# Kernel optimization log

Hardware: AMD Instinct MI355X
Metric: run time of the kernel (lower is better)

The kernel has to match this reference:

```python
import jax, jax.numpy as jnp
import numpy as np

WH, WW = 8, 8          # window size
NH = 8                 # num heads
ED = 256               # embed dim
HD = ED // NH          # head dim
SCALE = HD ** -0.5


def setup_inputs() -> dict:
    key = jax.random.key(0)
    k1, k2, k3, k4 = jax.random.split(key, 4)
    x = jax.random.normal(k1, (8, ED, 128, 128), dtype=jnp.float32)
    w_qkv = jax.random.normal(k2, (3 * ED, ED), dtype=jnp.float32) * (ED ** -0.5)
    w_out = jax.random.normal(k3, (ED, ED), dtype=jnp.float32) * (ED ** -0.5)
    b_out = jax.random.normal(k4, (ED,), dtype=jnp.float32) * 0.01
    return {"x": x, "w_qkv": w_qkv, "w_out": w_out, "b_out": b_out}


def reference(x, w_qkv, w_out, b_out):
    # x: [B, C, H, W] (NCHW) -> [B, H, W, C]
    x = jnp.transpose(x, (0, 2, 3, 1))
    B, H, W, C = x.shape
    pad_h = (WH - H % WH) % WH
    pad_w = (WW - W % WW) % WW
    x = jnp.pad(x, ((0, 0), (0, pad_h), (0, pad_w), (0, 0)))
    Hp, Wp = H + pad_h, W + pad_w
    nh, nw = Hp // WH, Wp // WW
    N = WH * WW
    # window partition -> [B*nh*nw, N, C]
    xw = x.reshape(B, nh, WH, nw, WW, C).transpose(0, 1, 3, 2, 4, 5).reshape(-1, N, C)
    # qkv projection (no bias): [nW, N, 3, NH, HD]
    qkv = (xw @ w_qkv.T).reshape(-1, N, 3, NH, HD)
    q, k, v = qkv[:, :, 0], qkv[:, :, 1], qkv[:, :, 2]  # [nW, N, NH, HD]
    # NOTE: faithful to source — attention across the HEADS axis per token
    attn = jnp.einsum('wnhd,wngd->wnhg', q, k) * SCALE  # [nW, N, NH, NH]
    attn = jax.nn.softmax(attn, axis=-1)
    out = jnp.einsum('wnhg,wngd->wnhd', attn, v)        # [nW, N, NH, HD]
    # torch: transpose(1,2).reshape(-1, N, C)
    out = out.transpose(0, 2, 1, 3).reshape(-1, N, C)
    out = out @ w_out.T + b_out
    # window merge
    out = out.reshape(B, nh, nw, WH, WW, C).transpose(0, 1, 3, 2, 4, 5).reshape(B, Hp, Wp, C)
    out = out[:, :H, :W, :]
    # faithful final permute(0,3,2,1): [B, C, W, H]
    return jnp.transpose(out, (0, 3, 2, 1))
```

## Files before the change

### kernel.cpp

```cpp
#include <hip/hip_runtime.h>

#define SCALE 0.17677669529663687f

typedef __attribute__((ext_vector_type(8))) short bf16x8;
typedef __attribute__((ext_vector_type(4))) float f32x4;

__device__ __forceinline__ unsigned short f2bf(float f) {
    unsigned u = __float_as_uint(f);
    u += 0x7FFFu + ((u >> 16) & 1u);
    return (unsigned short)(u >> 16);
}
__device__ __forceinline__ float bf2f(unsigned short s) {
    return __uint_as_float(((unsigned)s) << 16);
}

__global__ __launch_bounds__(256) void wconv_kernel(
        const float* __restrict__ w_qkv, const float* __restrict__ w_out,
        unsigned short* __restrict__ wq, unsigned short* __restrict__ wo) {
    int idx = blockIdx.x * 256 + threadIdx.x;
    if (idx < 196608) wq[idx] = f2bf(w_qkv[idx]);
    else if (idx < 262144) wo[idx - 196608] = f2bf(w_out[idx - 196608]);
}

__global__ __launch_bounds__(512, 4) void qkv_attn_kernel(
        const float* __restrict__ x, const unsigned short* __restrict__ wq,
        unsigned short* __restrict__ o_ws) {
    __shared__ unsigned char lds[65536];
    const int tid = threadIdx.x;
    const int bid = blockIdx.x;
    const int rpair = bid & 3;
    const int iwp   = (bid >> 2) & 7;
    const int ih    = (bid >> 5) & 15;
    const int b     = bid >> 9;
    const int r0 = rpair * 2;
    const float* xb2 = x + (size_t)b * 4194304 + (size_t)(ih * 8 + r0) * 128 + iwp * 16;

    #pragma unroll
    for (int it = 0; it < 4; ++it) {
        int idx = it * 512 + tid;
        int c_lo = idx & 7;
        int q4   = (idx >> 3) & 3;
        int c_hi = (idx >> 5) & 31;
        int rl   = idx >> 10;
        int c = c_hi * 8 + c_lo;
        float4 v = *(const float4*)(xb2 + (size_t)c * 16384 + rl * 128 + q4 * 4);
        #pragma unroll
        for (int j = 0; j < 4; ++j) {
            int t = rl * 16 + q4 * 4 + j;
            int slot = (c >> 3) ^ (t & 7);
            float f = (j == 0) ? v.x : (j == 1) ? v.y : (j == 2) ? v.z : v.w;
            *(unsigned short*)(lds + 49152 + t * 512 + (slot << 4) + (c & 7) * 2) = f2bf(f);
        }
    }
    __syncthreads();

    const int lane = tid & 63;
    const int wave = tid >> 6;
    const int lrow = lane & 15;
    const int lk   = lane >> 4;

    {
        const int j0 = wave * 96;
        f32x4 acc[2][6];
        #pragma unroll
        for (int mt = 0; mt < 2; ++mt)
            #pragma unroll
            for (int nt = 0; nt < 6; ++nt)
                acc[mt][nt] = (f32x4){0.f, 0.f, 0.f, 0.f};
        #pragma unroll
        for (int k = 0; k < 8; ++k) {
            bf16x8 a[2], bb[6];
            #pragma unroll
            for (int mt = 0; mt < 2; ++mt) {
                int t = mt * 16 + lrow;
                int slot = (k * 4 + lk) ^ (t & 7);
                a[mt] = *(const bf16x8*)(lds + 49152 + t * 512 + (slot << 4));
            }
            #pragma unroll
            for (int nt = 0; nt < 6; ++nt) {
                int j = j0 + nt * 16 + lrow;
                bb[nt] = *(const bf16x8*)((const unsigned char*)wq + (size_t)j * 512 + k * 64 + lk * 16);
            }
            #pragma unroll
            for (int mt = 0; mt < 2; ++mt)
                #pragma unroll
                for (int nt = 0; nt < 6; ++nt)
                    acc[mt][nt] = __builtin_amdgcn_mfma_f32_16x16x32_bf16(a[mt], bb[nt], acc[mt][nt], 0, 0, 0);
        }
        #pragma unroll
        for (int mt = 0; mt < 2; ++mt)
            #pragma unroll
            for (int nt = 0; nt < 6; ++nt)
                #pragma unroll
                for (int i = 0; i < 4; ++i) {
                    int t = mt * 16 + lk * 4 + i;
                    int ch = j0 + nt * 16 + lrow;
                    int slot = (ch >> 3) ^ (t & 7);
                    *(unsigned short*)(lds + t * 1536 + (slot << 4) + (ch & 7) * 2) = f2bf(acc[mt][nt][i]);
                }
    }
    __syncthreads();

    {
        const int t  = tid >> 4;
        const int h  = (tid >> 1) & 7;
        const int hf = tid & 1;
        const int tx = t & 7;
        const unsigned char* row = lds + t * 1536;
        float q[16];
        #pragma unroll
        for (int jj = 0; jj < 2; ++jj) {
            int slot = (h * 4 + hf * 2 + jj) ^ tx;
            bf16x8 v = *(const bf16x8*)(row + (slot << 4));
            #pragma unroll
            for (int e = 0; e < 8; ++e) q[jj * 8 + e] = bf2f((unsigned short)v[e]);
        }
        float dots[8];
        #pragma unroll
        for (int g = 0; g < 8; ++g) {
            float acc = 0.f;
            #pragma unroll
            for (int jj = 0; jj < 2; ++jj) {
                int slot = (32 + g * 4 + hf * 2 + jj) ^ tx;
                bf16x8 v = *(const bf16x8*)(row + (slot << 4));
                #pragma unroll
                for (int e = 0; e < 8; ++e) acc += q[jj * 8 + e] * bf2f((unsigned short)v[e]);
            }
            dots[g] = acc;
        }
        #pragma unroll
        for (int g = 0; g < 8; ++g)
            dots[g] = (dots[g] + __shfl_xor(dots[g], 1, 64)) * SCALE;
        float mx = dots[0];
        #pragma unroll
        for (int g = 1; g < 8; ++g) mx = fmaxf(mx, dots[g]);
        float sum = 0.f;
        #pragma unroll
        for (int g = 0; g < 8; ++g) { dots[g] = __expf(dots[g] - mx); sum += dots[g]; }
        float inv = 1.f / sum;
        float o[16];
        #pragma unroll
        for (int d = 0; d < 16; ++d) o[d] = 0.f;
        #pragma unroll
        for (int g = 0; g < 8; ++g) {
            float p = dots[g] * inv;
            #pragma unroll
            for (int jj = 0; jj < 2; ++jj) {
                int slot = (64 + g * 4 + hf * 2 + jj) ^ tx;
                bf16x8 v = *(const bf16x8*)(row + (slot << 4));
                #pragma unroll
                for (int e = 0; e < 8; ++e) o[jj * 8 + e] += p * bf2f((unsigned short)v[e]);
            }
        }
        const int rl = t >> 4, sg = t & 15;
        const int win = b * 256 + ih * 16 + iwp * 2 + (sg >> 3);
        const int r = r0 + rl, s = sg & 7;
        unsigned short* dst = o_ws + ((size_t)win * 64 + h * 8 + r) * 256 + s * 32 + hf * 16;
        #pragma unroll
        for (int jj = 0; jj < 2; ++jj) {
            bf16x8 pk;
            #pragma unroll
            for (int e = 0; e < 8; ++e) pk[e] = (short)f2bf(o[jj * 8 + e]);
            *(bf16x8*)(dst + jj * 8) = pk;
        }
    }
}

__global__ __launch_bounds__(512, 4) void outproj_kernel(
        const unsigned short* __restrict__ o_ws, const unsigned short* __restrict__ wo,
        const float* __restrict__ b_out, float* __restrict__ out) {
    __shared__ unsigned char lds[65536];
    const int tid = threadIdx.x;
    const int bid = blockIdx.x;
    const int b  = bid >> 8;
    const int ih = (bid >> 4) & 15;
    const int iw = bid & 15;

    {
        const unsigned char* src = (const unsigned char*)(o_ws + (size_t)bid * 16384);
        #pragma unroll
        for (int it = 0; it < 4; ++it) {
            int q = it * 512 + tid;
            int np = q >> 5;
            int slot = (q & 31) ^ (np & 7);
            *(bf16x8*)(lds + np * 512 + (slot << 4)) = *(const bf16x8*)(src + q * 16);
        }
    }
    __syncthreads();

    const int lane = tid & 63;
    const int wave = tid >> 6;
    const int lrow = lane & 15;
    const int lk   = lane >> 4;
    const int j0 = wave * 32;

    f32x4 acc[4][2];
    #pragma unroll
    for (int mt = 0; mt < 4; ++mt)
        #pragma unroll
        for (int nt = 0; nt < 2; ++nt)
            acc[mt][nt] = (f32x4){0.f, 0.f, 0.f, 0.f};
    #pragma unroll
    for (int k = 0; k < 8; ++k) {
        bf16x8 a[4], bb[2];
        #pragma unroll
        for (int mt = 0; mt < 4; ++mt) {
            int t = mt * 16 + lrow;
            int slot = (k * 4 + lk) ^ (t & 7);
            a[mt] = *(const bf16x8*)(lds + t * 512 + (slot << 4));
        }
        #pragma unroll
        for (int nt = 0; nt < 2; ++nt) {
            int j = j0 + nt * 16 + lrow;
            bb[nt] = *(const bf16x8*)((const unsigned char*)wo + (size_t)j * 512 + k * 64 + lk * 16);
        }
        #pragma unroll
        for (int mt = 0; mt < 4; ++mt)
            #pragma unroll
            for (int nt = 0; nt < 2; ++nt)
                acc[mt][nt] = __builtin_amdgcn_mfma_f32_16x16x32_bf16(a[mt], bb[nt], acc[mt][nt], 0, 0, 0);
    }
    float bias[2];
    #pragma unroll
    for (int nt = 0; nt < 2; ++nt) bias[nt] = b_out[j0 + nt * 16 + lrow];
    __syncthreads();
    #pragma unroll
    for (int mt = 0; mt < 4; ++mt)
        #pragma unroll
        for (int nt = 0; nt < 2; ++nt)
            #pragma unroll
            for (int i = 0; i < 4; ++i) {
                int t = mt * 16 + lk * 4 + i;
                int e = j0 + nt * 16 + lrow;
                int sl = (e >> 2) ^ (t & 7);
                *(float*)(lds + t * 1024 + (sl << 4) + (e & 3) * 4) = acc[mt][nt][i] + bias[nt];
            }
    __syncthreads();
    const size_t obase = ((size_t)b * 256) * 16384 + (size_t)(iw * 8) * 128 + ih * 8;
    #pragma unroll
    for (int it = 0; it < 4; ++it) {
        int idx = it * 512 + tid;
        int e = idx >> 3, sp = idx & 7;
        float vals[8];
        #pragma unroll
        for (int rp = 0; rp < 8; ++rp) {
            int t = rp * 8 + sp;
            int sl = (e >> 2) ^ (t & 7);
            vals[rp] = *(const float*)(lds + t * 1024 + (sl << 4) + (e & 3) * 4);
        }
        float* po = out + obase + (size_t)e * 16384 + sp * 128;
        *(float4*)po       = make_float4(vals[0], vals[1], vals[2], vals[3]);
        *(float4*)(po + 4) = make_float4(vals[4], vals[5], vals[6], vals[7]);
    }
}

extern "C" void kernel_launch(void* const* d_in, const int* in_sizes, int n_in,
                              void* d_out, int out_size, void* d_ws, size_t ws_size,
                              hipStream_t stream) {
    const float* x     = (const float*)d_in[0];
    const float* w_qkv = (const float*)d_in[1];
    const float* w_out = (const float*)d_in[2];
    const float* b_out = (const float*)d_in[3];
    float* out = (float*)d_out;

    unsigned short* o_ws = (unsigned short*)d_ws;
    unsigned short* wq   = (unsigned short*)((char*)d_ws + 67108864);
    unsigned short* wo   = wq + 196608;

    wconv_kernel<<<dim3(1024), dim3(256), 0, stream>>>(w_qkv, w_out, wq, wo);
    qkv_attn_kernel<<<dim3(4096), dim3(512), 0, stream>>>(x, wq, o_ws);
    outproj_kernel<<<dim3(2048), dim3(512), 0, stream>>>(o_ws, wo, b_out, out);
}
```

Baseline: 292.0 us.

## Split fused QKV+attention into separate GEMM and attention kernels when workspace allows

When the workspace is large enough, the fused qkv_attn kernel is replaced by a standalone QKV GEMM kernel that writes a bf16 QKV buffer (about 200 MB), followed by a separate per-token attention kernel. The output projection kernel is also reworked to use half the LDS, writing results back in two halves, and its occupancy hint is raised. The intent is higher occupancy and simpler kernels, at the cost of an extra round trip of the large QKV tensor through global memory. The original fused path is kept as a fallback for small workspaces.

```diff
diff --git a/kernel.cpp b/kernel.cpp
--- a/kernel.cpp
+++ b/kernel.cpp
@@ -20,6 +20,266 @@
     int idx = blockIdx.x * 256 + threadIdx.x;
     if (idx < 196608) wq[idx] = f2bf(w_qkv[idx]);
     else if (idx < 262144) wo[idx - 196608] = f2bf(w_out[idx - 196608]);
+}
+
+
+__global__ __launch_bounds__(512, 4) void qkv_gemm_kernel(
+        const float* __restrict__ x, const unsigned short* __restrict__ wq,
+        unsigned short* __restrict__ qkv_ws) {
+    __shared__ unsigned char lds[65536];
+    const int tid = threadIdx.x;
+    const int tb  = blockIdx.x << 6;
+    const int b   = tb >> 14;
+    const int hw  = tb & 16383;
+    const float* xb = x + (size_t)b * 4194304 + hw;
+
+    #pragma unroll
+    for (int it = 0; it < 8; ++it) {
+        int idx = it * 512 + tid;
+        int c = idx >> 4, q4 = idx & 15;
+        float4 v = *(const float4*)(xb + (size_t)c * 16384 + q4 * 4);
+        #pragma unroll
+        for (int j = 0; j < 4; ++j) {
+            int t = q4 * 4 + j;
+            int slot = (c >> 3) ^ (t & 7);
+            float f = (j == 0) ? v.x : (j == 1) ? v.y : (j == 2) ? v.z : v.w;
+            *(unsigned short*)(lds + t * 512 + (slot << 4) + (c & 7) * 2) = f2bf(f);
+        }
+    }
+    __syncthreads();
+
+    const int lane = tid & 63, wave = tid >> 6;
+    const int lrow = lane & 15, lk = lane >> 4;
+    const int j0w = wave * 32;
+
+    for (int nb = 0; nb < 3; ++nb) {
+        f32x4 acc[4][2];
+        #pragma unroll
+        for (int mt = 0; mt < 4; ++mt)
+            #pragma unroll
+            for (int nt = 0; nt < 2; ++nt)
+                acc[mt][nt] = (f32x4){0.f, 0.f, 0.f, 0.f};
+        #pragma unroll
+        for (int k = 0; k < 8; ++k) {
+            bf16x8 a[4], bb[2];
+            #pragma unroll
+            for (int mt = 0; mt < 4; ++mt) {
+                int t = mt * 16 + lrow;
+                int slot = (k * 4 + lk) ^ (t & 7);
+                a[mt] = *(const bf16x8*)(lds + t * 512 + (slot << 4));
+            }
+            #pragma unroll
+            for (int nt = 0; nt < 2; ++nt) {
+                int j = nb * 256 + j0w + nt * 16 + lrow;
+                bb[nt] = *(const bf16x8*)((const unsigned char*)wq + (size_t)j * 512 + k * 64 + lk * 16);
+            }
+            #pragma unroll
+            for (int mt = 0; mt < 4; ++mt)
+                #pragma unroll
+                for (int nt = 0; nt < 2; ++nt)
+                    acc[mt][nt] = __builtin_amdgcn_mfma_f32_16x16x32_bf16(a[mt], bb[nt], acc[mt][nt], 0, 0, 0);
+        }
+        #pragma unroll
+        for (int mt = 0; mt < 4; ++mt)
+            #pragma unroll
+            for (int nt = 0; nt < 2; ++nt)
+                #pragma unroll
+                for (int i = 0; i < 4; ++i) {
+                    int t = mt * 16 + lk * 4 + i;
+                    int ch = j0w + nt * 16 + lrow;
+                    int slot = (ch >> 3) ^ (t & 7);
+                    *(unsigned short*)(lds + 32768 + t * 512 + (slot << 4) + (ch & 7) * 2) = f2bf(acc[mt][nt][i]);
+                }
+        __syncthreads();
+        #pragma unroll
+        for (int it = 0; it < 4; ++it) {
+            int idx = it * 512 + tid;
+            int t = idx >> 5, c = idx & 31;
+            int slot = c ^ (t & 7);
+            bf16x8 vch = *(const bf16x8*)(lds + 32768 + t * 512 + (slot << 4));
+            *(bf16x8*)(qkv_ws + (size_t)(tb + t) * 768 + nb * 256 + c * 8) = vch;
+        }
+        __syncthreads();
+    }
+}
+
+__global__ __launch_bounds__(512, 6) void attn_kernel(
+        const unsigned short* __restrict__ qkv_ws, unsigned short* __restrict__ o_ws) {
+    __shared__ unsigned char lds[49152];
+    const int tid = threadIdx.x;
+    const int tb  = blockIdx.x << 5;
+
+    {
+        const int t = tid >> 4, cpart = tid & 15;
+        const unsigned short* src = qkv_ws + (size_t)(tb + t) * 768;
+        #pragma unroll
+        for (int ci = 0; ci < 6; ++ci) {
+            int c = ci * 16 + cpart;
+            *(bf16x8*)(lds + t * 1536 + ((c ^ (t & 7)) << 4)) = *(const bf16x8*)(src + c * 8);
+        }
+    }
+    __syncthreads();
+
+    const int t  = tid >> 4;
+    const int h  = (tid >> 1) & 7;
+    const int hf = tid & 1;
+    const int tx = t & 7;
+    const unsigned char* row = lds + t * 1536;
+    float q[16];
+    #pragma unroll
+    for (int jj = 0; jj < 2; ++jj) {
+        int slot = (h * 4 + hf * 2 + jj) ^ tx;
+        bf16x8 v = *(const bf16x8*)(row + (slot << 4));
+        #pragma unroll
+        for (int e = 0; e < 8; ++e) q[jj * 8 + e] = bf2f((unsigned short)v[e]);
+    }
+    float dots[8];
+    #pragma unroll
+    for (int g = 0; g < 8; ++g) {
+        float acc = 0.f;
+        #pragma unroll
+        for (int jj = 0; jj < 2; ++jj) {
+            int slot = (32 + g * 4 + hf * 2 + jj) ^ tx;
+            bf16x8 v = *(const bf16x8*)(row + (slot << 4));
+            #pragma unroll
+            for (int e = 0; e < 8; ++e) acc += q[jj * 8 + e] * bf2f((unsigned short)v[e]);
+        }
+        dots[g] = acc;
+    }
+    #pragma unroll
+    for (int g = 0; g < 8; ++g)
+        dots[g] = (dots[g] + __shfl_xor(dots[g], 1, 64)) * SCALE;
+    float mx = dots[0];
+    #pragma unroll
+    for (int g = 1; g < 8; ++g) mx = fmaxf(mx, dots[g]);
+    float sum = 0.f;
+    #pragma unroll
+    for (int g = 0; g < 8; ++g) { dots[g] = __expf(dots[g] - mx); sum += dots[g]; }
+    float inv = 1.f / sum;
+    float o[16];
+    #pragma unroll
+    for (int d = 0; d < 16; ++d) o[d] = 0.f;
+    #pragma unroll
+    for (int g = 0; g < 8; ++g) {
+        float p = dots[g] * inv;
+        #pragma unroll
+        for (int jj = 0; jj < 2; ++jj) {
+            int slot = (64 + g * 4 + hf * 2 + jj) ^ tx;
+            bf16x8 v = *(const bf16x8*)(row + (slot << 4));
+            #pragma unroll
+            for (int e = 0; e < 8; ++e) o[jj * 8 + e] += p * bf2f((unsigned short)v[e]);
+        }
+    }
+    const int tok = tb + t;
+    const int bb2 = tok >> 14, rem = tok & 16383;
+    const int himg = rem >> 7, wimg = rem & 127;
+    const int ih = himg >> 3, r = himg & 7;
+    const int iw = wimg >> 3, s = wimg & 7;
+    const int win = (bb2 << 8) + (ih << 4) + iw;
+    unsigned short* dst = o_ws + ((size_t)win * 64 + h * 8 + r) * 256 + s * 32 + hf * 16;
+    #pragma unroll
+    for (int jj = 0; jj < 2; ++jj) {
+        bf16x8 pk;
+        #pragma unroll
+        for (int e = 0; e < 8; ++e) pk[e] = (short)f2bf(o[jj * 8 + e]);
+        *(bf16x8*)(dst + jj * 8) = pk;
+    }
+}
+
+__global__ __launch_bounds__(512, 6) void outproj_kernel(
+        const unsigned short* __restrict__ o_ws, const unsigned short* __restrict__ wo,
+        const float* __restrict__ b_out, float* __restrict__ out) {
+    __shared__ unsigned char lds[32768];
+    const int tid = threadIdx.x;
+    const int bid = blockIdx.x;
+    const int b  = bid >> 8;
+    const int ih = (bid >> 4) & 15;
+    const int iw = bid & 15;
+
+    {
+        const unsigned char* src = (const unsigned char*)(o_ws + (size_t)bid * 16384);
+        #pragma unroll
+        for (int it = 0; it < 4; ++it) {
+            int q = it * 512 + tid;
+            int np = q >> 5;
+            int slot = (q & 31) ^ (np & 7);
+            *(bf16x8*)(lds + np * 512 + (slot << 4)) = *(const bf16x8*)(src + q * 16);
+        }
+    }
+    __syncthreads();
+
+    const int lane = tid & 63;
+    const int wave = tid >> 6;
+    const int lrow = lane & 15;
+    const int lk   = lane >> 4;
+    const int j0 = wave * 32;
+
+    f32x4 acc[4][2];
+    #pragma unroll
+    for (int mt = 0; mt < 4; ++mt)
+        #pragma unroll
+        for (int nt = 0; nt < 2; ++nt)
+            acc[mt][nt] = (f32x4){0.f, 0.f, 0.f, 0.f};
+    #pragma unroll
+    for (int k = 0; k < 8; ++k) {
+        bf16x8 a[4], bb[2];
+        #pragma unroll
+        for (int mt = 0; mt < 4; ++mt) {
+            int t = mt * 16 + lrow;
+            int slot = (k * 4 + lk) ^ (t & 7);
+            a[mt] = *(const bf16x8*)(lds + t * 512 + (slot << 4));
+        }
+        #pragma unroll
+        for (int nt = 0; nt < 2; ++nt) {
+            int j = j0 + nt * 16 + lrow;
+            bb[nt] = *(const bf16x8*)((const unsigned char*)wo + (size_t)j * 512 + k * 64 + lk * 16);
+        }
+        #pragma unroll
+        for (int mt = 0; mt < 4; ++mt)
+            #pragma unroll
+            for (int nt = 0; nt < 2; ++nt)
+                acc[mt][nt] = __builtin_amdgcn_mfma_f32_16x16x32_bf16(a[mt], bb[nt], acc[mt][nt], 0, 0, 0);
+    }
+    float bias[2];
+    #pragma unroll
+    for (int nt = 0; nt < 2; ++nt) bias[nt] = b_out[j0 + nt * 16 + lrow];
+    __syncthreads();
+
+    const size_t obase = ((size_t)b * 256) * 16384 + (size_t)(iw * 8) * 128 + ih * 8;
+    #pragma unroll
+    for (int half = 0; half < 2; ++half) {
+        if ((wave >> 2) == half) {
+            int jl = (wave & 3) * 32;
+            #pragma unroll
+            for (int mt = 0; mt < 4; ++mt)
+                #pragma unroll
+                for (int nt = 0; nt < 2; ++nt)
+                    #pragma unroll
+                    for (int i = 0; i < 4; ++i) {
+                        int t = mt * 16 + lk * 4 + i;
+                        int el = jl + nt * 16 + lrow;
+                        int sl = (el >> 2) ^ (t & 7);
+                        *(float*)(lds + t * 512 + (sl << 4) + (el & 3) * 4) = acc[mt][nt][i] + bias[nt];
+                    }
+        }
+        __syncthreads();
+        #pragma unroll
+        for (int it = 0; it < 2; ++it) {
+            int idx = it * 512 + tid;
+            int el = idx >> 3, sp = idx & 7;
+            float vals[8];
+            #pragma unroll
+            for (int rp = 0; rp < 8; ++rp) {
+                int t = rp * 8 + sp;
+                int sl = (el >> 2) ^ (t & 7);
+                vals[rp] = *(const float*)(lds + t * 512 + (sl << 4) + (el & 3) * 4);
+            }
+            float* po = out + obase + (size_t)(half * 128 + el) * 16384 + sp * 128;
+            *(float4*)po       = make_float4(vals[0], vals[1], vals[2], vals[3]);
+            *(float4*)(po + 4) = make_float4(vals[4], vals[5], vals[6], vals[7]);
+        }
+        __syncthreads();
+    }
 }
 
 __global__ __launch_bounds__(512, 4) void qkv_attn_kernel(
@@ -166,94 +426,6 @@
     }
 }
 
-__global__ __launch_bounds__(512, 4) void outproj_kernel(
-        const unsigned short* __restrict__ o_ws, const unsigned short* __restrict__ wo,
-        const float* __restrict__ b_out, float* __restrict__ out) {
-    __shared__ unsigned char lds[65536];
-    const int tid = threadIdx.x;
-    const int bid = blockIdx.x;
-    const int b  = bid >> 8;
-    const int ih = (bid >> 4) & 15;
-    const int iw = bid & 15;
-
-    {
-        const unsigned char* src = (const unsigned char*)(o_ws + (size_t)bid * 16384);
-        #pragma unroll
-        for (int it = 0; it < 4; ++it) {
-            int q = it * 512 + tid;
-            int np = q >> 5;
-            int slot = (q & 31) ^ (np & 7);
-            *(bf16x8*)(lds + np * 512 + (slot << 4)) = *(const bf16x8*)(src + q * 16);
-        }
-    }
-    __syncthreads();
-
-    const int lane = tid & 63;
-    const int wave = tid >> 6;
-    const int lrow = lane & 15;
-    const int lk   = lane >> 4;
-    const int j0 = wave * 32;
-
-    f32x4 acc[4][2];
-    #pragma unroll
-    for (int mt = 0; mt < 4; ++mt)
-        #pragma unroll
-        for (int nt = 0; nt < 2; ++nt)
-            acc[mt][nt] = (f32x4){0.f, 0.f, 0.f, 0.f};
-    #pragma unroll
-    for (int k = 0; k < 8; ++k) {
-        bf16x8 a[4], bb[2];
-        #pragma unroll
-        for (int mt = 0; mt < 4; ++mt) {
-            int t = mt * 16 + lrow;
-            int slot = (k * 4 + lk) ^ (t & 7);
-            a[mt] = *(const bf16x8*)(lds + t * 512 + (slot << 4));
-        }
-        #pragma unroll
-        for (int nt = 0; nt < 2; ++nt) {
-            int j = j0 + nt * 16 + lrow;
-            bb[nt] = *(const bf16x8*)((const unsigned char*)wo + (size_t)j * 512 + k * 64 + lk * 16);
-        }
-        #pragma unroll
-        for (int mt = 0; mt < 4; ++mt)
-            #pragma unroll
-            for (int nt = 0; nt < 2; ++nt)
-                acc[mt][nt] = __builtin_amdgcn_mfma_f32_16x16x32_bf16(a[mt], bb[nt], acc[mt][nt], 0, 0, 0);
-    }
-    float bias[2];
-    #pragma unroll
-    for (int nt = 0; nt < 2; ++nt) bias[nt] = b_out[j0 + nt * 16 + lrow];
-    __syncthreads();
-    #pragma unroll
-    for (int mt = 0; mt < 4; ++mt)
-        #pragma unroll
-        for (int nt = 0; nt < 2; ++nt)
-            #pragma unroll
-            for (int i = 0; i < 4; ++i) {
-                int t = mt * 16 + lk * 4 + i;
-                int e = j0 + nt * 16 + lrow;
-                int sl = (e >> 2) ^ (t & 7);
-                *(float*)(lds + t * 1024 + (sl << 4) + (e & 3) * 4) = acc[mt][nt][i] + bias[nt];
-            }
-    __syncthreads();
-    const size_t obase = ((size_t)b * 256) * 16384 + (size_t)(iw * 8) * 128 + ih * 8;
-    #pragma unroll
-    for (int it = 0; it < 4; ++it) {
-        int idx = it * 512 + tid;
-        int e = idx >> 3, sp = idx & 7;
-        float vals[8];
-        #pragma unroll
-        for (int rp = 0; rp < 8; ++rp) {
-            int t = rp * 8 + sp;
-            int sl = (e >> 2) ^ (t & 7);
-            vals[rp] = *(const float*)(lds + t * 1024 + (sl << 4) + (e & 3) * 4);
-        }
-        float* po = out + obase + (size_t)e * 16384 + sp * 128;
-        *(float4*)po       = make_float4(vals[0], vals[1], vals[2], vals[3]);
-        *(float4*)(po + 4) = make_float4(vals[4], vals[5], vals[6], vals[7]);
-    }
-}
-
 extern "C" void kernel_launch(void* const* d_in, const int* in_sizes, int n_in,
                               void* d_out, int out_size, void* d_ws, size_t ws_size,
                               hipStream_t stream) {
@@ -263,11 +435,24 @@
     const float* b_out = (const float*)d_in[3];
     float* out = (float*)d_out;
 
-    unsigned short* o_ws = (unsigned short*)d_ws;
-    unsigned short* wq   = (unsigned short*)((char*)d_ws + 67108864);
-    unsigned short* wo   = wq + 196608;
-
-    wconv_kernel<<<dim3(1024), dim3(256), 0, stream>>>(w_qkv, w_out, wq, wo);
-    qkv_attn_kernel<<<dim3(4096), dim3(512), 0, stream>>>(x, wq, o_ws);
-    outproj_kernel<<<dim3(2048), dim3(512), 0, stream>>>(o_ws, wo, b_out, out);
-}
+    const size_t QKV_BYTES = 201326592;
+    const size_t O_BYTES   = 67108864;
+
+    if (ws_size >= QKV_BYTES + O_BYTES + 786432) {
+        unsigned short* qkv_ws = (unsigned short*)d_ws;
+        unsigned short* o_ws   = (unsigned short*)((char*)d_ws + QKV_BYTES);
+        unsigned short* wq     = (unsigned short*)((char*)d_ws + QKV_BYTES + O_BYTES);
+        unsigned short* wo     = wq + 196608;
+        wconv_kernel<<<dim3(1024), dim3(256), 0, stream>>>(w_qkv, w_out, wq, wo);
+        qkv_gemm_kernel<<<dim3(2048), dim3(512), 0, stream>>>(x, wq, qkv_ws);
+        attn_kernel<<<dim3(4096), dim3(512), 0, stream>>>(qkv_ws, o_ws);
+        outproj_kernel<<<dim3(2048), dim3(512), 0, stream>>>(o_ws, wo, b_out, out);
+    } else {
+        unsigned short* o_ws = (unsigned short*)d_ws;
+        unsigned short* wq   = (unsigned short*)((char*)d_ws + O_BYTES);
+        unsigned short* wo   = wq + 196608;
+        wconv_kernel<<<dim3(1024), dim3(256), 0, stream>>>(w_qkv, w_out, wq, wo);
+        qkv_attn_kernel<<<dim3(4096), dim3(512), 0, stream>>>(x, wq, o_ws);
+        outproj_kernel<<<dim3(2048), dim3(512), 0, stream>>>(o_ws, wo, b_out, out);
+    }
+}
```

New measurement: 309.8 us. 1.06x slower.

## Split fused QKV-attention kernel into separate GEMM and attention kernels

Applied to the files above, without the earlier changes.

Replaces the fused QKV projection plus per-token head attention kernel with two kernels. A token-tiled bf16 MFMA GEMM writes the full QKV tensor to a global workspace, and a separate attention kernel reads it back. The output projection kernel now stages its result in two halves through a smaller LDS buffer and raises its occupancy bound. The intent is smaller LDS footprints and better occupancy, at the cost of a large extra global round trip for the QKV intermediate.

```diff
diff --git a/kernel.cpp b/kernel.cpp
--- a/kernel.cpp
+++ b/kernel.cpp
@@ -12,6 +12,9 @@
 }
 __device__ __forceinline__ float bf2f(unsigned short s) {
     return __uint_as_float(((unsigned)s) << 16);
+}
+__device__ __forceinline__ unsigned pk2c(float a, float b) {
+    return (unsigned)f2bf(a) | ((unsigned)f2bf(b) << 16);
 }
 
 __global__ __launch_bounds__(256) void wconv_kernel(
@@ -22,154 +25,144 @@
     else if (idx < 262144) wo[idx - 196608] = f2bf(w_out[idx - 196608]);
 }
 
-__global__ __launch_bounds__(512, 4) void qkv_attn_kernel(
+__global__ __launch_bounds__(256, 4) void qkv_gemm_kernel(
         const float* __restrict__ x, const unsigned short* __restrict__ wq,
-        unsigned short* __restrict__ o_ws) {
-    __shared__ unsigned char lds[65536];
+        unsigned short* __restrict__ qkv_ws) {
+    __shared__ unsigned char lds[32768];
+    const int tid  = threadIdx.x;
+    const int tb   = blockIdx.x << 6;
+    const int b    = tb >> 14;
+    const int hw0  = tb & 16383;
+    const float* xb = x + (size_t)b * 4194304 + hw0;
+    const int tok  = tid & 63;
+    const int wave = tid >> 6;
+
+    #pragma unroll
+    for (int cg = 0; cg < 8; ++cg) {
+        const int c0 = wave * 64 + cg * 8;
+        float f[8];
+        #pragma unroll
+        for (int e = 0; e < 8; ++e) f[e] = xb[(size_t)(c0 + e) * 16384 + tok];
+        unsigned u0 = pk2c(f[0], f[1]), u1 = pk2c(f[2], f[3]);
+        unsigned u2 = pk2c(f[4], f[5]), u3 = pk2c(f[6], f[7]);
+        const int slot = (c0 >> 3) ^ (tok & 7);
+        *(uint4*)(lds + tok * 512 + (slot << 4)) = make_uint4(u0, u1, u2, u3);
+    }
+    __syncthreads();
+
+    const int lane = tid & 63;
+    const int lrow = lane & 15, lk = lane >> 4;
+
+    for (int nb = 0; nb < 3; ++nb) {
+        const int ch0 = nb * 256 + wave * 64;
+        f32x4 acc[4][4];
+        #pragma unroll
+        for (int mt = 0; mt < 4; ++mt)
+            #pragma unroll
+            for (int nt = 0; nt < 4; ++nt)
+                acc[mt][nt] = (f32x4){0.f, 0.f, 0.f, 0.f};
+        #pragma unroll
+        for (int k = 0; k < 8; ++k) {
+            bf16x8 aw[4], bx[4];
+            #pragma unroll
+            for (int mt = 0; mt < 4; ++mt)
+                aw[mt] = *(const bf16x8*)((const unsigned char*)wq +
+                        (size_t)(ch0 + mt * 16 + lrow) * 512 + k * 64 + lk * 16);
+            #pragma unroll
+            for (int nt = 0; nt < 4; ++nt) {
+                int t = nt * 16 + lrow;
+                int slot = (k * 4 + lk) ^ (t & 7);
+                bx[nt] = *(const bf16x8*)(lds + t * 512 + (slot << 4));
+            }
+            #pragma unroll
+            for (int mt = 0; mt < 4; ++mt)
+                #pragma unroll
+                for (int nt = 0; nt < 4; ++nt)
+                    acc[mt][nt] = __builtin_amdgcn_mfma_f32_16x16x32_bf16(aw[mt], bx[nt], acc[mt][nt], 0, 0, 0);
+        }
+        #pragma unroll
+        for (int nt = 0; nt < 4; ++nt) {
+            const size_t tokg = tb + nt * 16 + lrow;
+            #pragma unroll
+            for (int mt = 0; mt < 4; ++mt) {
+                const int ch = ch0 + mt * 16 + lk * 4;
+                uint2 v;
+                v.x = pk2c(acc[mt][nt][0], acc[mt][nt][1]);
+                v.y = pk2c(acc[mt][nt][2], acc[mt][nt][3]);
+                *(uint2*)(qkv_ws + tokg * 768 + ch) = v;
+            }
+        }
+    }
+}
+
+__global__ __launch_bounds__(256, 4) void attn_kernel(
+        const unsigned short* __restrict__ qkv_ws, unsigned short* __restrict__ o_ws) {
     const int tid = threadIdx.x;
-    const int bid = blockIdx.x;
-    const int rpair = bid & 3;
-    const int iwp   = (bid >> 2) & 7;
-    const int ih    = (bid >> 5) & 15;
-    const int b     = bid >> 9;
-    const int r0 = rpair * 2;
-    const float* xb2 = x + (size_t)b * 4194304 + (size_t)(ih * 8 + r0) * 128 + iwp * 16;
-
-    #pragma unroll
-    for (int it = 0; it < 4; ++it) {
-        int idx = it * 512 + tid;
-        int c_lo = idx & 7;
-        int q4   = (idx >> 3) & 3;
-        int c_hi = (idx >> 5) & 31;
-        int rl   = idx >> 10;
-        int c = c_hi * 8 + c_lo;
-        float4 v = *(const float4*)(xb2 + (size_t)c * 16384 + rl * 128 + q4 * 4);
-        #pragma unroll
-        for (int j = 0; j < 4; ++j) {
-            int t = rl * 16 + q4 * 4 + j;
-            int slot = (c >> 3) ^ (t & 7);
-            float f = (j == 0) ? v.x : (j == 1) ? v.y : (j == 2) ? v.z : v.w;
-            *(unsigned short*)(lds + 49152 + t * 512 + (slot << 4) + (c & 7) * 2) = f2bf(f);
-        }
-    }
-    __syncthreads();
-
-    const int lane = tid & 63;
-    const int wave = tid >> 6;
-    const int lrow = lane & 15;
-    const int lk   = lane >> 4;
-
-    {
-        const int j0 = wave * 96;
-        f32x4 acc[2][6];
-        #pragma unroll
-        for (int mt = 0; mt < 2; ++mt)
-            #pragma unroll
-            for (int nt = 0; nt < 6; ++nt)
-                acc[mt][nt] = (f32x4){0.f, 0.f, 0.f, 0.f};
-        #pragma unroll
-        for (int k = 0; k < 8; ++k) {
-            bf16x8 a[2], bb[6];
-            #pragma unroll
-            for (int mt = 0; mt < 2; ++mt) {
-                int t = mt * 16 + lrow;
-                int slot = (k * 4 + lk) ^ (t & 7);
-                a[mt] = *(const bf16x8*)(lds + 49152 + t * 512 + (slot << 4));
-            }
-            #pragma unroll
-            for (int nt = 0; nt < 6; ++nt) {
-                int j = j0 + nt * 16 + lrow;
-                bb[nt] = *(const bf16x8*)((const unsigned char*)wq + (size_t)j * 512 + k * 64 + lk * 16);
-            }
-            #pragma unroll
-            for (int mt = 0; mt < 2; ++mt)
-                #pragma unroll
-                for (int nt = 0; nt < 6; ++nt)
-                    acc[mt][nt] = __builtin_amdgcn_mfma_f32_16x16x32_bf16(a[mt], bb[nt], acc[mt][nt], 0, 0, 0);
-        }
-        #pragma unroll
-        for (int mt = 0; mt < 2; ++mt)
-            #pragma unroll
-            for (int nt = 0; nt < 6; ++nt)
-                #pragma unroll
-                for (int i = 0; i < 4; ++i) {
-                    int t = mt * 16 + lk * 4 + i;
-                    int ch = j0 + nt * 16 + lrow;
-                    int slot = (ch >> 3) ^ (t & 7);
-                    *(unsigned short*)(lds + t * 1536 + (slot << 4) + (ch & 7) * 2) = f2bf(acc[mt][nt][i]);
-                }
-    }
-    __syncthreads();
-
-    {
-        const int t  = tid >> 4;
-        const int h  = (tid >> 1) & 7;
-        const int hf = tid & 1;
-        const int tx = t & 7;
-        const unsigned char* row = lds + t * 1536;
-        float q[16];
+    const int tok = (blockIdx.x << 4) + (tid >> 4);
+    const int h   = (tid >> 1) & 7;
+    const int hf  = tid & 1;
+    const unsigned short* row = qkv_ws + (size_t)tok * 768;
+
+    float q[16];
+    #pragma unroll
+    for (int jj = 0; jj < 2; ++jj) {
+        bf16x8 v = *(const bf16x8*)(row + h * 32 + hf * 16 + jj * 8);
+        #pragma unroll
+        for (int e = 0; e < 8; ++e) q[jj * 8 + e] = bf2f((unsigned short)v[e]);
+    }
+    float dots[8];
+    #pragma unroll
+    for (int g = 0; g < 8; ++g) {
+        float acc = 0.f;
         #pragma unroll
         for (int jj = 0; jj < 2; ++jj) {
-            int slot = (h * 4 + hf * 2 + jj) ^ tx;
-            bf16x8 v = *(const bf16x8*)(row + (slot << 4));
-            #pragma unroll
-            for (int e = 0; e < 8; ++e) q[jj * 8 + e] = bf2f((unsigned short)v[e]);
-        }
-        float dots[8];
-        #pragma unroll
-        for (int g = 0; g < 8; ++g) {
-            float acc = 0.f;
-            #pragma unroll
-            for (int jj = 0; jj < 2; ++jj) {
-                int slot = (32 + g * 4 + hf * 2 + jj) ^ tx;
-                bf16x8 v = *(const bf16x8*)(row + (slot << 4));
-                #pragma unroll
-                for (int e = 0; e < 8; ++e) acc += q[jj * 8 + e] * bf2f((unsigned short)v[e]);
-            }
-            dots[g] = acc;
-        }
-        #pragma unroll
-        for (int g = 0; g < 8; ++g)
-            dots[g] = (dots[g] + __shfl_xor(dots[g], 1, 64)) * SCALE;
-        float mx = dots[0];
-        #pragma unroll
-        for (int g = 1; g < 8; ++g) mx = fmaxf(mx, dots[g]);
-        float sum = 0.f;
-        #pragma unroll
-        for (int g = 0; g < 8; ++g) { dots[g] = __expf(dots[g] - mx); sum += dots[g]; }
-        float inv = 1.f / sum;
-        float o[16];
-        #pragma unroll
-        for (int d = 0; d < 16; ++d) o[d] = 0.f;
-        #pragma unroll
-        for (int g = 0; g < 8; ++g) {
-            float p = dots[g] * inv;
-            #pragma unroll
-            for (int jj = 0; jj < 2; ++jj) {
-                int slot = (64 + g * 4 + hf * 2 + jj) ^ tx;
-                bf16x8 v = *(const bf16x8*)(row + (slot << 4));
-                #pragma unroll
-                for (int e = 0; e < 8; ++e) o[jj * 8 + e] += p * bf2f((unsigned short)v[e]);
-            }
-        }
-        const int rl = t >> 4, sg = t & 15;
-        const int win = b * 256 + ih * 16 + iwp * 2 + (sg >> 3);
-        const int r = r0 + rl, s = sg & 7;
-        unsigned short* dst = o_ws + ((size_t)win * 64 + h * 8 + r) * 256 + s * 32 + hf * 16;
+            bf16x8 v = *(const bf16x8*)(row + 256 + g * 32 + hf * 16 + jj * 8);
+            #pragma unroll
+            for (int e = 0; e < 8; ++e) acc += q[jj * 8 + e] * bf2f((unsigned short)v[e]);
+        }
+        dots[g] = acc;
+    }
+    #pragma unroll
+    for (int g = 0; g < 8; ++g)
+        dots[g] = (dots[g] + __shfl_xor(dots[g], 1, 64)) * SCALE;
+    float mx = dots[0];
+    #pragma unroll
+    for (int g = 1; g < 8; ++g) mx = fmaxf(mx, dots[g]);
+    float sum = 0.f;
+    #pragma unroll
+    for (int g = 0; g < 8; ++g) { dots[g] = __expf(dots[g] - mx); sum += dots[g]; }
+    const float inv = 1.f / sum;
+    float o[16];
+    #pragma unroll
+    for (int d = 0; d < 16; ++d) o[d] = 0.f;
+    #pragma unroll
+    for (int g = 0; g < 8; ++g) {
+        const float p = dots[g] * inv;
         #pragma unroll
         for (int jj = 0; jj < 2; ++jj) {
-            bf16x8 pk;
-            #pragma unroll
-            for (int e = 0; e < 8; ++e) pk[e] = (short)f2bf(o[jj * 8 + e]);
-            *(bf16x8*)(dst + jj * 8) = pk;
-        }
-    }
-}
-
-__global__ __launch_bounds__(512, 4) void outproj_kernel(
+            bf16x8 v = *(const bf16x8*)(row + 512 + g * 32 + hf * 16 + jj * 8);
+            #pragma unroll
+            for (int e = 0; e < 8; ++e) o[jj * 8 + e] += p * bf2f((unsigned short)v[e]);
+        }
+    }
+    const int bb2 = tok >> 14, rem = tok & 16383;
+    const int himg = rem >> 7, wimg = rem & 127;
+    const int ih = himg >> 3, r = himg & 7;
+    const int iw = wimg >> 3, s = wimg & 7;
+    const int win = (bb2 << 8) + (ih << 4) + iw;
+    unsigned short* dst = o_ws + ((size_t)win * 64 + h * 8 + r) * 256 + s * 32 + hf * 16;
+    #pragma unroll
+    for (int jj = 0; jj < 2; ++jj) {
+        uint4 v = make_uint4(pk2c(o[jj * 8 + 0], o[jj * 8 + 1]), pk2c(o[jj * 8 + 2], o[jj * 8 + 3]),
+                             pk2c(o[jj * 8 + 4], o[jj * 8 + 5]), pk2c(o[jj * 8 + 6], o[jj * 8 + 7]));
+        *(uint4*)(dst + jj * 8) = v;
+    }
+}
+
+__global__ __launch_bounds__(512, 6) void outproj_kernel(
         const unsigned short* __restrict__ o_ws, const unsigned short* __restrict__ wo,
         const float* __restrict__ b_out, float* __restrict__ out) {
-    __shared__ unsigned char lds[65536];
+    __shared__ unsigned char lds[32768];
     const int tid = threadIdx.x;
     const int bid = blockIdx.x;
     const int b  = bid >> 8;
@@ -224,33 +217,41 @@
     #pragma unroll
     for (int nt = 0; nt < 2; ++nt) bias[nt] = b_out[j0 + nt * 16 + lrow];
     __syncthreads();
-    #pragma unroll
-    for (int mt = 0; mt < 4; ++mt)
-        #pragma unroll
-        for (int nt = 0; nt < 2; ++nt)
-            #pragma unroll
-            for (int i = 0; i < 4; ++i) {
-                int t = mt * 16 + lk * 4 + i;
-                int e = j0 + nt * 16 + lrow;
-                int sl = (e >> 2) ^ (t & 7);
-                *(float*)(lds + t * 1024 + (sl << 4) + (e & 3) * 4) = acc[mt][nt][i] + bias[nt];
+
+    const size_t obase = ((size_t)b * 256) * 16384 + (size_t)(iw * 8) * 128 + ih * 8;
+    #pragma unroll
+    for (int half = 0; half < 2; ++half) {
+        if ((wave >> 2) == half) {
+            int jl = (wave & 3) * 32;
+            #pragma unroll
+            for (int mt = 0; mt < 4; ++mt)
+                #pragma unroll
+                for (int nt = 0; nt < 2; ++nt)
+                    #pragma unroll
+                    for (int i = 0; i < 4; ++i) {
+                        int t = mt * 16 + lk * 4 + i;
+                        int el = jl + nt * 16 + lrow;
+                        int sl = (el >> 2) ^ (t & 7);
+                        *(float*)(lds + t * 512 + (sl << 4) + (el & 3) * 4) = acc[mt][nt][i] + bias[nt];
+                    }
+        }
+        __syncthreads();
+        #pragma unroll
+        for (int it = 0; it < 2; ++it) {
+            int idx = it * 512 + tid;
+            int el = idx >> 3, sp = idx & 7;
+            float vals[8];
+            #pragma unroll
+            for (int rp = 0; rp < 8; ++rp) {
+                int t = rp * 8 + sp;
+                int sl = (el >> 2) ^ (t & 7);
+                vals[rp] = *(const float*)(lds + t * 512 + (sl << 4) + (el & 3) * 4);
             }
-    __syncthreads();
-    const size_t obase = ((size_t)b * 256) * 16384 + (size_t)(iw * 8) * 128 + ih * 8;
-    #pragma unroll
-    for (int it = 0; it < 4; ++it) {
-        int idx = it * 512 + tid;
-        int e = idx >> 3, sp = idx & 7;
-        float vals[8];
-        #pragma unroll
-        for (int rp = 0; rp < 8; ++rp) {
-            int t = rp * 8 + sp;
-            int sl = (e >> 2) ^ (t & 7);
-            vals[rp] = *(const float*)(lds + t * 1024 + (sl << 4) + (e & 3) * 4);
-        }
-        float* po = out + obase + (size_t)e * 16384 + sp * 128;
-        *(float4*)po       = make_float4(vals[0], vals[1], vals[2], vals[3]);
-        *(float4*)(po + 4) = make_float4(vals[4], vals[5], vals[6], vals[7]);
+            float* po = out + obase + (size_t)(half * 128 + el) * 16384 + sp * 128;
+            *(float4*)po       = make_float4(vals[0], vals[1], vals[2], vals[3]);
+            *(float4*)(po + 4) = make_float4(vals[4], vals[5], vals[6], vals[7]);
+        }
+        __syncthreads();
     }
 }
 
@@ -263,11 +264,16 @@
     const float* b_out = (const float*)d_in[3];
     float* out = (float*)d_out;
 
-    unsigned short* o_ws = (unsigned short*)d_ws;
-    unsigned short* wq   = (unsigned short*)((char*)d_ws + 67108864);
-    unsigned short* wo   = wq + 196608;
+    const size_t QKV_BYTES = 201326592;
+    const size_t O_BYTES   = 67108864;
+
+    unsigned short* qkv_ws = (unsigned short*)d_ws;
+    unsigned short* o_ws   = (unsigned short*)((char*)d_ws + QKV_BYTES);
+    unsigned short* wq     = (unsigned short*)((char*)d_ws + QKV_BYTES + O_BYTES);
+    unsigned short* wo     = wq + 196608;
 
     wconv_kernel<<<dim3(1024), dim3(256), 0, stream>>>(w_qkv, w_out, wq, wo);
-    qkv_attn_kernel<<<dim3(4096), dim3(512), 0, stream>>>(x, wq, o_ws);
+    qkv_gemm_kernel<<<dim3(2048), dim3(256), 0, stream>>>(x, wq, qkv_ws);
+    attn_kernel<<<dim3(8192), dim3(256), 0, stream>>>(qkv_ws, o_ws);
     outproj_kernel<<<dim3(2048), dim3(512), 0, stream>>>(o_ws, wo, b_out, out);
 }
```

New measurement: 428.4 us. 1.47x slower.
